# Kernel tuning notes

Hardware: AMD Instinct MI355X
Metric: run time of the kernel (lower is better)

The kernel has to match this reference:

```python
import jax, jax.numpy as jnp
import numpy as np

N = 50000      # nodes
E = 800000     # edges
G = 256        # graphs in batch
D_IN = 128     # input_dim
H = 128        # node_hidden_dim
FC = 128       # fc_hidden_dim
OUT = 2        # out_dim
EPS = 1e-5


def _lin_init(key, fan_in, fan_out, bias=True):
    kw, kb = jax.random.split(key)
    w = jax.random.normal(kw, (fan_in, fan_out), jnp.float32) / np.sqrt(fan_in)
    if bias:
        b = jax.random.normal(kb, (fan_out,), jnp.float32) * 0.01
        return w, b
    return w


def setup_inputs() -> dict:
    key = jax.random.key(0)
    ks = jax.random.split(key, 16)
    x = jax.random.normal(ks[0], (N, D_IN), jnp.float32)
    edge_index = jax.random.randint(ks[1], (2, E), 0, N, jnp.int32)
    batch = jnp.sort(jax.random.randint(ks[2], (N,), 0, G, jnp.int32))
    edge_attr = jax.random.uniform(ks[3], (E, 1), jnp.float32)
    # GraphConv params: lin_rel (with bias) + lin_root (no bias)
    w_rel1, b_rel1 = _lin_init(ks[4], D_IN, H)
    w_root1 = _lin_init(ks[5], D_IN, H, bias=False)
    w_rel2, b_rel2 = _lin_init(ks[6], H, 2 * H)
    w_root2 = _lin_init(ks[7], H, 2 * H, bias=False)
    w_rel3, b_rel3 = _lin_init(ks[8], 2 * H, 3 * H)
    w_root3 = _lin_init(ks[9], 2 * H, 3 * H, bias=False)
    # BatchNorm affine params
    gamma1 = jnp.ones((H,), jnp.float32);      beta1 = jnp.zeros((H,), jnp.float32)
    gamma2 = jnp.ones((2 * H,), jnp.float32);  beta2 = jnp.zeros((2 * H,), jnp.float32)
    gamma3 = jnp.ones((3 * H,), jnp.float32);  beta3 = jnp.zeros((3 * H,), jnp.float32)
    # FC head: lin1 in = 3H+6H+9H = 18H
    w_lin1, b_lin1 = _lin_init(ks[10], 18 * H, FC)
    w_lin2, b_lin2 = _lin_init(ks[11], FC, OUT)
    w_lin3, b_lin3 = _lin_init(ks[12], OUT, OUT)
    return dict(x=x, edge_index=edge_index, batch=batch, edge_attr=edge_attr,
                w_rel1=w_rel1, b_rel1=b_rel1, w_root1=w_root1,
                w_rel2=w_rel2, b_rel2=b_rel2, w_root2=w_root2,
                w_rel3=w_rel3, b_rel3=b_rel3, w_root3=w_root3,
                gamma1=gamma1, beta1=beta1, gamma2=gamma2, beta2=beta2,
                gamma3=gamma3, beta3=beta3,
                w_lin1=w_lin1, b_lin1=b_lin1, w_lin2=w_lin2, b_lin2=b_lin2,
                w_lin3=w_lin3, b_lin3=b_lin3)


def _bn(h, gamma, beta):
    # training-mode BatchNorm1d over node axis
    mu = h.mean(0)
    var = h.var(0)
    return (h - mu) * jax.lax.rsqrt(var + EPS) * gamma + beta


def _gconv(h, src, dst, ew, w_rel, b_rel, w_root):
    # PyG GraphConv: lin_rel(sum_j ew_ij * x_j) + lin_root(x_i)
    agg = jax.ops.segment_sum(h[src] * ew[:, None], dst, num_segments=N)
    return agg @ w_rel + b_rel + h @ w_root


def _pool3(h, batch):
    # concat of global max / mean / add pooling per graph
    s = jax.ops.segment_sum(h, batch, num_segments=G)
    cnt = jax.ops.segment_sum(jnp.ones((h.shape[0], 1), h.dtype), batch, num_segments=G)
    mean = s / jnp.maximum(cnt, 1.0)
    m = jax.ops.segment_max(h, batch, num_segments=G)
    m = jnp.where(cnt > 0, m, 0.0)  # guard empty segments
    return jnp.concatenate([m, mean, s], axis=1)


def reference(x, edge_index, batch, edge_attr,
              w_rel1, b_rel1, w_root1, w_rel2, b_rel2, w_root2,
              w_rel3, b_rel3, w_root3,
              gamma1, beta1, gamma2, beta2, gamma3, beta3,
              w_lin1, b_lin1, w_lin2, b_lin2, w_lin3, b_lin3):
    ew = jnp.transpose(edge_attr, (1, 0))[0]            # [E]
    src, dst = edge_index[0], edge_index[1]
    h = _bn(jax.nn.leaky_relu(_gconv(x, src, dst, ew, w_rel1, b_rel1, w_root1)), gamma1, beta1)
    x1 = _pool3(h, batch)
    h = _bn(jax.nn.leaky_relu(_gconv(h, src, dst, ew, w_rel2, b_rel2, w_root2)), gamma2, beta2)
    x2 = _pool3(h, batch)
    h = _bn(jax.nn.leaky_relu(_gconv(h, src, dst, ew, w_rel3, b_rel3, w_root3)), gamma3, beta3)
    x3 = _pool3(h, batch)
    z = jnp.concatenate([x1, x2, x3], axis=1)           # [G, 18H]
    z = jax.nn.relu(z @ w_lin1 + b_lin1)                # dropout is identity in eval
    z = jax.nn.relu(z @ w_lin2 + b_lin2)
    return jax.nn.log_softmax(z @ w_lin3 + b_lin3, axis=-1)
```

## Files before the change

kernel.cpp:

```cpp
#include <hip/hip_runtime.h>
#include <cstdint>
#include <cstddef>

#define N_NODES 50000
#define M_PAD   50048
#define MB_TILES 391
#define N_EDGES 800000
#define N_GRAPH 256
#define Z_DIM   2304
#define NREP    16
#define POOL_TOT (N_GRAPH * (128 + 256 + 384))

static constexpr float LEAKY  = 0.01f;
static constexpr float BN_EPS = 1e-5f;

typedef short short8 __attribute__((ext_vector_type(8)));
typedef float floatx4 __attribute__((ext_vector_type(4)));
typedef const __attribute__((address_space(1))) unsigned int* gas_ptr;
typedef __attribute__((address_space(3))) unsigned int* las_ptr;
typedef unsigned long long ull;

__device__ __forceinline__ unsigned short f2b(float f) {
  union { float f; unsigned int u; } v; v.f = f;
  unsigned int u = v.u;
  unsigned int r = (u + 0x7FFFu + ((u >> 16) & 1u)) >> 16;
  return (unsigned short)r;
}
__device__ __forceinline__ float b2f(unsigned short h) {
  union { unsigned int u; float f; } v; v.u = ((unsigned int)h) << 16;
  return v.f;
}
__device__ __forceinline__ unsigned fkey(float x) {
  unsigned k = __float_as_uint(x);
  return k ^ ((k & 0x80000000u) ? 0xFFFFFFFFu : 0x80000000u);
}
__device__ __forceinline__ float kdec(unsigned k) {
  k ^= (k & 0x80000000u) ? 0x80000000u : 0xFFFFFFFFu;
  return __uint_as_float(k);
}


__global__ void init_all_kernel(int* __restrict__ cntR, int* __restrict__ gcnt,
                                float* __restrict__ sums_all,
                                unsigned* __restrict__ pmaxk, unsigned* __restrict__ pmink,
                                float* __restrict__ psumg) {
  const int i = blockIdx.x * blockDim.x + threadIdx.x;
  if (i < NREP * N_NODES) cntR[i] = 0;
  if (i < N_GRAPH) gcnt[i] = 0;
  if (i < 2 * (128 + 256 + 384)) sums_all[i] = 0.f;
  if (i < POOL_TOT) { pmaxk[i] = 0u; pmink[i] = 0xFFFFFFFFu; psumg[i] = 0.f; }
}


__global__ void hist_rep_kernel(const int* __restrict__ idx, int* __restrict__ cntR, int n) {
  int i = blockIdx.x * blockDim.x + threadIdx.x;
  if (i < n) {
    const int rep = blockIdx.x & (NREP - 1);
    atomicAdd(&cntR[rep * N_NODES + idx[i]], 1);
  }
}

__global__ __launch_bounds__(256) void scan1_fused_kernel(int* __restrict__ cntR,
                                                          int* __restrict__ out,
                                                          int* __restrict__ part, int n) {
  __shared__ int sm[256];
  const int t = threadIdx.x;
  const int base = blockIdx.x * 1024 + t * 4;
  int v[4] = {0, 0, 0, 0};
#pragma unroll
  for (int j = 0; j < 4; ++j) {
    const int d = base + j;
    if (d < n) {
      int s = 0;
#pragma unroll
      for (int r = 0; r < NREP; ++r) {
        const int c = cntR[r * N_NODES + d];
        cntR[r * N_NODES + d] = s;
        s += c;
      }
      v[j] = s;
    }
  }
  const int tsum = v[0] + v[1] + v[2] + v[3];
  sm[t] = tsum;
  __syncthreads();
  for (int off = 1; off < 256; off <<= 1) {
    int x = (t >= off) ? sm[t - off] : 0;
    __syncthreads();
    sm[t] += x;
    __syncthreads();
  }
  const int excl = sm[t] - tsum;
  if (base     < n) out[base]     = excl;
  if (base + 1 < n) out[base + 1] = excl + v[0];
  if (base + 2 < n) out[base + 2] = excl + v[0] + v[1];
  if (base + 3 < n) out[base + 3] = excl + v[0] + v[1] + v[2];
  if (t == 255) part[blockIdx.x] = sm[255];
}

__global__ __launch_bounds__(256) void scan2_kernel(int* __restrict__ part, int nb,
                                                    int* __restrict__ total_out) {
  __shared__ int sm[256];
  const int t = threadIdx.x;
  const int v = (t < nb) ? part[t] : 0;
  sm[t] = v;
  __syncthreads();
  for (int off = 1; off < 256; off <<= 1) {
    int x = (t >= off) ? sm[t - off] : 0;
    __syncthreads();
    sm[t] += x;
    __syncthreads();
  }
  if (t < nb) part[t] = sm[t] - v;
  if (t == 255) *total_out = sm[255];
}

__global__ void scan3_cursor_kernel(int* __restrict__ out, const int* __restrict__ part,
                                    int* __restrict__ cntR, int n) {
  int i = blockIdx.x * blockDim.x + threadIdx.x;
  if (i >= n) return;
  const int rp = out[i] + part[i >> 10];
  out[i] = rp;
#pragma unroll
  for (int r = 0; r < NREP; ++r) cntR[r * N_NODES + i] += rp;
}

__global__ void bucket_kernel(const int* __restrict__ src, const int* __restrict__ dst,
                              const float* __restrict__ ew, int* __restrict__ cntR,
                              ull* __restrict__ epack, int E) {
  int e = blockIdx.x * blockDim.x + threadIdx.x;
  if (e < E) {
    const int rep = blockIdx.x & (NREP - 1);
    const int d = dst[e];
    const int p = atomicAdd(&cntR[rep * N_NODES + d], 1);
    epack[p] = ((ull)__float_as_uint(ew[e]) << 32) | (unsigned)src[e];
  }
}

__global__ __launch_bounds__(256) void hist_batch_kernel(const int* __restrict__ idx,
                                                         int* __restrict__ cnt, int n) {
  __shared__ int lh[N_GRAPH];
  lh[threadIdx.x] = 0;
  __syncthreads();
  int i = blockIdx.x * blockDim.x + threadIdx.x;
  if (i < n) atomicAdd(&lh[idx[i]], 1);
  __syncthreads();
  const int v = lh[threadIdx.x];
  if (v) atomicAdd(&cnt[threadIdx.x], v);
}

__global__ __launch_bounds__(256) void scan256_kernel(const int* __restrict__ cnt,
                                                      int* __restrict__ gptr) {
  __shared__ int sm[256];
  const int t = threadIdx.x;
  const int v = cnt[t];
  sm[t] = v;
  __syncthreads();
  for (int off = 1; off < 256; off <<= 1) {
    int x = (t >= off) ? sm[t - off] : 0;
    __syncthreads();
    sm[t] += x;
    __syncthreads();
  }
  gptr[t] = sm[t] - v;
  if (t == 255) gptr[256] = sm[255];
}


__global__ void cast_bf16_kernel(const float* __restrict__ in,
                                 unsigned short* __restrict__ out, int npair) {
  int i = blockIdx.x * blockDim.x + threadIdx.x;
  if (i >= npair) return;
  float2 v = *(const float2*)(in + 2 * (size_t)i);
  ((unsigned int*)out)[i] = (unsigned int)f2b(v.x) | ((unsigned int)f2b(v.y) << 16);
}

__global__ __launch_bounds__(256) void wt_build_kernel(
    const float* __restrict__ wrel, const float* __restrict__ wroot,
    const float* __restrict__ brel, const float* __restrict__ sums_prev,
    const float* __restrict__ gamma_prev, const float* __restrict__ beta_prev,
    unsigned short* __restrict__ wt, float* __restrict__ u, float* __restrict__ v,
    int K, int N) {
  __shared__ float redu[256];
  __shared__ float redv[256];
  const int n = blockIdx.x;
  const int K2 = 2 * K;
  const float inv_n = 1.f / (float)N_NODES;
  float us = 0.f, vs = 0.f;
  for (int k = threadIdx.x; k < K2; k += 256) {
    const int kk = (k < K) ? k : k - K;
    const float w = (k < K) ? wrel[(size_t)kk * N + n] : wroot[(size_t)kk * N + n];
    float sc = 1.f, sh = 0.f;
    if (sums_prev) {
      const float mu  = sums_prev[kk] * inv_n;
      const float var = sums_prev[K + kk] * inv_n - mu * mu;
      sc = rsqrtf(var + BN_EPS) * gamma_prev[kk];
      sh = beta_prev[kk] - mu * sc;
    }
    wt[(size_t)n * K2 + k] = f2b(w * sc);
    if (k < K) us += sh * w; else vs += sh * w;
  }
  redu[threadIdx.x] = us; redv[threadIdx.x] = vs;
  __syncthreads();
  for (int o = 128; o > 0; o >>= 1) {
    if (threadIdx.x < o) {
      redu[threadIdx.x] += redu[threadIdx.x + o];
      redv[threadIdx.x] += redv[threadIdx.x + o];
    }
    __syncthreads();
  }
  if (threadIdx.x == 0) { u[n] = redu[0]; v[n] = brel[n] + redv[0]; }
}


template <int D>
__global__ void agg_bf16_kernel(const unsigned short* __restrict__ h,
                                const int* __restrict__ rowptr,
                                const ull* __restrict__ epack,
                                unsigned short* __restrict__ agg,
                                float* __restrict__ degw_out) {
  int gid  = blockIdx.x * blockDim.x + threadIdx.x;
  int node = gid >> 6;
  int lane = threadIdx.x & 63;
  if (node >= N_NODES) return;
  const int beg = rowptr[node], end = rowptr[node + 1];
  constexpr int NP = D / 128;
  float acc0[NP], acc1[NP];
#pragma unroll
  for (int i = 0; i < NP; ++i) { acc0[i] = 0.f; acc1[i] = 0.f; }
  float wsum = 0.f;

  int p = beg;
  for (; p + 4 <= end; p += 4) {
    const ull p0 = epack[p],     p1 = epack[p + 1];
    const ull p2 = epack[p + 2], p3 = epack[p + 3];
    const int s0 = (int)(unsigned)p0, s1 = (int)(unsigned)p1;
    const int s2 = (int)(unsigned)p2, s3 = (int)(unsigned)p3;
    const float w0 = __uint_as_float((unsigned)(p0 >> 32));
    const float w1 = __uint_as_float((unsigned)(p1 >> 32));
    const float w2 = __uint_as_float((unsigned)(p2 >> 32));
    const float w3 = __uint_as_float((unsigned)(p3 >> 32));
    wsum += w0 + w1 + w2 + w3;
    const unsigned int* r0 = (const unsigned int*)(h + (size_t)s0 * D);
    const unsigned int* r1 = (const unsigned int*)(h + (size_t)s1 * D);
    const unsigned int* r2 = (const unsigned int*)(h + (size_t)s2 * D);
    const unsigned int* r3 = (const unsigned int*)(h + (size_t)s3 * D);
    unsigned int u0[NP], u1[NP], u2[NP], u3[NP];
#pragma unroll
    for (int i = 0; i < NP; ++i) {
      u0[i] = r0[lane + 64 * i];
      u1[i] = r1[lane + 64 * i];
      u2[i] = r2[lane + 64 * i];
      u3[i] = r3[lane + 64 * i];
    }
#pragma unroll
    for (int i = 0; i < NP; ++i) {
      acc0[i] += b2f((unsigned short)(u0[i] & 0xFFFF)) * w0
               + b2f((unsigned short)(u1[i] & 0xFFFF)) * w1
               + b2f((unsigned short)(u2[i] & 0xFFFF)) * w2
               + b2f((unsigned short)(u3[i] & 0xFFFF)) * w3;
      acc1[i] += b2f((unsigned short)(u0[i] >> 16)) * w0
               + b2f((unsigned short)(u1[i] >> 16)) * w1
               + b2f((unsigned short)(u2[i] >> 16)) * w2
               + b2f((unsigned short)(u3[i] >> 16)) * w3;
    }
  }
  for (; p < end; ++p) {
    const ull pk = epack[p];
    const int   s = (int)(unsigned)pk;
    const float w = __uint_as_float((unsigned)(pk >> 32));
    wsum += w;
    const unsigned int* row = (const unsigned int*)(h + (size_t)s * D);
#pragma unroll
    for (int i = 0; i < NP; ++i) {
      unsigned int uu = row[lane + 64 * i];
      acc0[i] += b2f((unsigned short)(uu & 0xFFFF)) * w;
      acc1[i] += b2f((unsigned short)(uu >> 16)) * w;
    }
  }
  unsigned int* o = (unsigned int*)(agg + (size_t)node * D);
#pragma unroll
  for (int i = 0; i < NP; ++i)
    o[lane + 64 * i] = (unsigned int)f2b(acc0[i]) | ((unsigned int)f2b(acc1[i]) << 16);
  if (degw_out != nullptr && lane == 0) degw_out[node] = wsum;
}


__global__ __launch_bounds__(256) void gemm_mfma_kernel(
    const unsigned short* __restrict__ Aagg, const unsigned short* __restrict__ Ah,
    const unsigned short* __restrict__ Wt,
    const float* __restrict__ u, const float* __restrict__ v,
    const float* __restrict__ degw,
    unsigned short* __restrict__ outH, float* __restrict__ sums,
    int M, int K, int N) {
  __shared__ unsigned short As[128 * 32];
  __shared__ unsigned short Bs[128 * 32];
  __shared__ float col_s[256];
  __shared__ float dws[128];

  const int NT = N >> 7;
  const int id = blockIdx.x;
  const int xcd = id & 7;
  const int q   = id >> 3;
  const int m_tile = (q / NT) * 8 + xcd;
  if (m_tile >= MB_TILES) return;
  const int m0 = m_tile * 128;
  const int n0 = (q % NT) * 128;

  const int t  = threadIdx.x;
  const int lane = t & 63;
  const int w    = t >> 6;
  const int wm   = (w & 1) * 64;
  const int wn   = (w >> 1) * 64;
  const int l16  = lane & 15;
  const int lq   = lane >> 4;
  const int K2   = 2 * K;

  const int lrow  = lane >> 2;
  const int lslot = lane & 3;

  col_s[t] = 0.f;
  if (t < 128) {
    const int m = m0 + t;
    dws[t] = (m < M) ? degw[m] : 0.f;
  }

  floatx4 acc[4][4];
#pragma unroll
  for (int i = 0; i < 4; ++i)
#pragma unroll
    for (int j = 0; j < 4; ++j) acc[i][j] = (floatx4){0.f, 0.f, 0.f, 0.f};

  for (int k0 = 0; k0 < K2; k0 += 32) {
    const unsigned short* Asrc;
    int kbase;
    if (k0 < K) { Asrc = Aagg; kbase = k0; } else { Asrc = Ah; kbase = k0 - K; }

    __syncthreads();
#pragma unroll
    for (int qq = 0; qq < 2; ++qq) {
      const int row = w * 32 + qq * 16 + lrow;
      const int gc  = (lslot ^ ((row >> 1) & 3)) * 8;
      const unsigned short* gA = Asrc + (size_t)(m0 + row) * K + kbase + gc;
      const unsigned short* gB = Wt + (size_t)(n0 + row) * K2 + k0 + gc;
      __builtin_amdgcn_global_load_lds((gas_ptr)gA, (las_ptr)(As + (w * 32 + qq * 16) * 32),
                                       16, 0, 0);
      __builtin_amdgcn_global_load_lds((gas_ptr)gB, (las_ptr)(Bs + (w * 32 + qq * 16) * 32),
                                       16, 0, 0);
    }
    __syncthreads();

    short8 af[4], bfr[4];
#pragma unroll
    for (int i = 0; i < 4; ++i) {
      const int r = wm + i * 16 + l16;
      af[i] = *(const short8*)(As + r * 32 + (lq ^ ((r >> 1) & 3)) * 8);
    }
#pragma unroll
    for (int j = 0; j < 4; ++j) {
      const int r = wn + j * 16 + l16;
      bfr[j] = *(const short8*)(Bs + r * 32 + (lq ^ ((r >> 1) & 3)) * 8);
    }

#pragma unroll
    for (int i = 0; i < 4; ++i)
#pragma unroll
      for (int j = 0; j < 4; ++j)
        acc[i][j] = __builtin_amdgcn_mfma_f32_16x16x32_bf16(af[i], bfr[j], acc[i][j], 0, 0, 0);
  }

  float uu[4], vv[4];
#pragma unroll
  for (int j = 0; j < 4; ++j) {
    const int n = n0 + wn + j * 16 + l16;
    uu[j] = u[n]; vv[j] = v[n];
  }

  float ts[4]  = {0.f, 0.f, 0.f, 0.f};
  float tss[4] = {0.f, 0.f, 0.f, 0.f};
#pragma unroll
  for (int i = 0; i < 4; ++i) {
    const int lrow2 = wm + i * 16 + lq * 4;
#pragma unroll
    for (int j = 0; j < 4; ++j) {
      const int n = n0 + wn + j * 16 + l16;
#pragma unroll
      for (int r = 0; r < 4; ++r) {
        const int m = m0 + lrow2 + r;
        if (m < M) {
          float val = acc[i][j][r] + vv[j] + dws[lrow2 + r] * uu[j];
          val = val > 0.f ? val : LEAKY * val;
          outH[(size_t)m * N + n] = f2b(val);
          ts[j]  += val;
          tss[j] += val * val;
        }
      }
    }
  }
#pragma unroll
  for (int j = 0; j < 4; ++j) {
    float a = ts[j], b = tss[j];
    a += __shfl_xor(a, 16); a += __shfl_xor(a, 32);
    b += __shfl_xor(b, 16); b += __shfl_xor(b, 32);
    if (lq == 0) {
      const int ci = wn + j * 16 + l16;
      atomicAdd(&col_s[ci], a);
      atomicAdd(&col_s[128 + ci], b);
    }
  }
  __syncthreads();
  if (t < 128) {
    atomicAdd(&sums[n0 + t], col_s[t]);
    atomicAdd(&sums[N + n0 + t], col_s[128 + t]);
  }
}


__global__ void pool_bf16_kernel(const unsigned short* __restrict__ hp,
                                 const int* __restrict__ batch,
                                 unsigned* __restrict__ pmaxk, unsigned* __restrict__ pmink,
                                 float* __restrict__ psumg, int n, int C) {
  __shared__ int bs[64];
  const int tc = threadIdx.x;
  const int r0 = blockIdx.x * 64;
  const int r1 = min(n, r0 + 64);
  if (tc < 64 && r0 + tc < n) bs[tc] = batch[r0 + tc];
  __syncthreads();
  int cur_g = bs[0];
  float mx0 = -3.4e38f, mn0 = 3.4e38f, s0 = 0.f;
  float mx1 = -3.4e38f, mn1 = 3.4e38f, s1 = 0.f;
  for (int r = r0; r < r1; ++r) {
    const int g = bs[r - r0];
    if (g != cur_g) {
      const int c0 = 2 * tc;
      atomicMax(&pmaxk[(size_t)cur_g * C + c0], fkey(mx0));
      atomicMin(&pmink[(size_t)cur_g * C + c0], fkey(mn0));
      atomicAdd(&psumg[(size_t)cur_g * C + c0], s0);
      atomicMax(&pmaxk[(size_t)cur_g * C + c0 + 1], fkey(mx1));
      atomicMin(&pmink[(size_t)cur_g * C + c0 + 1], fkey(mn1));
      atomicAdd(&psumg[(size_t)cur_g * C + c0 + 1], s1);
      mx0 = -3.4e38f; mn0 = 3.4e38f; s0 = 0.f;
      mx1 = -3.4e38f; mn1 = 3.4e38f; s1 = 0.f;
      cur_g = g;
    }
    const unsigned uu = ((const unsigned*)(hp + (size_t)r * C))[tc];
    const float a = b2f((unsigned short)(uu & 0xFFFF));
    const float b = b2f((unsigned short)(uu >> 16));
    mx0 = fmaxf(mx0, a); mn0 = fminf(mn0, a); s0 += a;
    mx1 = fmaxf(mx1, b); mn1 = fminf(mn1, b); s1 += b;
  }
  const int c0 = 2 * tc;
  atomicMax(&pmaxk[(size_t)cur_g * C + c0], fkey(mx0));
  atomicMin(&pmink[(size_t)cur_g * C + c0], fkey(mn0));
  atomicAdd(&psumg[(size_t)cur_g * C + c0], s0);
  atomicMax(&pmaxk[(size_t)cur_g * C + c0 + 1], fkey(mx1));
  atomicMin(&pmink[(size_t)cur_g * C + c0 + 1], fkey(mn1));
  atomicAdd(&psumg[(size_t)cur_g * C + c0 + 1], s1);
}


__global__ void pool_finalize_all_kernel(const unsigned* __restrict__ pmaxk,
                                         const unsigned* __restrict__ pmink,
                                         const float* __restrict__ psumg,
                                         const float* __restrict__ sums_all,
                                         const float* __restrict__ gamma1, const float* __restrict__ beta1,
                                         const float* __restrict__ gamma2, const float* __restrict__ beta2,
                                         const float* __restrict__ gamma3, const float* __restrict__ beta3,
                                         const int* __restrict__ gptr,
                                         float* __restrict__ z) {
  int i = blockIdx.x * blockDim.x + threadIdx.x;
  if (i >= POOL_TOT) return;
  int C, zoff, li;
  const float *sums, *gamma, *beta;
  if (i < N_GRAPH * 128) {
    C = 128; zoff = 0; li = i;
    sums = sums_all; gamma = gamma1; beta = beta1;
  } else if (i < N_GRAPH * (128 + 256)) {
    C = 256; zoff = 384; li = i - N_GRAPH * 128;
    sums = sums_all + 2 * 128; gamma = gamma2; beta = beta2;
  } else {
    C = 384; zoff = 1152; li = i - N_GRAPH * (128 + 256);
    sums = sums_all + 2 * (128 + 256); gamma = gamma3; beta = beta3;
  }
  const int g = li / C, c = li % C;
  const int cnt = gptr[g + 1] - gptr[g];
  const float inv_n = 1.f / (float)N_NODES;
  const float mu  = sums[c] * inv_n;
  const float var = sums[C + c] * inv_n - mu * mu;
  const float sc  = rsqrtf(var + BN_EPS) * gamma[c];
  const float sh  = beta[c] - mu * sc;
  const float mx = kdec(pmaxk[i]);
  const float mn = kdec(pmink[i]);
  const float sm = psumg[i];
  const float zmax = (sc >= 0.f ? mx : mn) * sc + sh;
  const float zsum = sm * sc + (float)cnt * sh;
  float* zg = z + (size_t)g * Z_DIM + zoff;
  zg[c]         = (cnt > 0) ? zmax : 0.f;
  zg[C + c]     = zsum / (float)(cnt > 0 ? cnt : 1);
  zg[2 * C + c] = zsum;
}


__global__ __launch_bounds__(1024) void fc_kernel(const float* __restrict__ z,
                                                  const float* __restrict__ w1, const float* __restrict__ b1,
                                                  const float* __restrict__ w2, const float* __restrict__ b2,
                                                  const float* __restrict__ w3, const float* __restrict__ b3,
                                                  float* __restrict__ out) {
  __shared__ float zs[Z_DIM];
  __shared__ float part[8][128];
  __shared__ float h1s[128];
  __shared__ float red[128][2];
  __shared__ float y2[2];
  const int g  = blockIdx.x;
  const int t  = threadIdx.x;
  const int c  = t & 127;
  const int ks = t >> 7;
  for (int i = t; i < Z_DIM; i += 1024) zs[i] = z[(size_t)g * Z_DIM + i];
  __syncthreads();

  constexpr int KCH = Z_DIM / 8;
  const int k0 = ks * KCH;
  float acc = 0.f;
#pragma unroll 4
  for (int k = k0; k < k0 + KCH; ++k) acc += zs[k] * w1[(size_t)k * 128 + c];
  part[ks][c] = acc;
  __syncthreads();

  if (t < 128) {
    float s = b1[t];
#pragma unroll
    for (int i = 0; i < 8; ++i) s += part[i][t];
    h1s[t] = fmaxf(s, 0.f);
  }
  __syncthreads();
  if (t < 128) {
    red[t][0] = h1s[t] * w2[t * 2 + 0];
    red[t][1] = h1s[t] * w2[t * 2 + 1];
  }
  __syncthreads();
  if (t < 2) {
    float s = b2[t];
    for (int k = 0; k < 128; ++k) s += red[k][t];
    y2[t] = fmaxf(s, 0.f);
  }
  __syncthreads();
  if (t == 0) {
    const float z0 = y2[0] * w3[0] + y2[1] * w3[2] + b3[0];
    const float z1 = y2[0] * w3[1] + y2[1] * w3[3] + b3[1];
    const float m  = fmaxf(z0, z1);
    const float lse = m + logf(expf(z0 - m) + expf(z1 - m));
    out[g * 2 + 0] = z0 - lse;
    out[g * 2 + 1] = z1 - lse;
  }
}


extern "C" void kernel_launch(void* const* d_in, const int* in_sizes, int n_in,
                              void* d_out, int out_size, void* d_ws, size_t ws_size,
                              hipStream_t stream) {
  (void)in_sizes; (void)n_in; (void)out_size; (void)ws_size;
  const float* x        = (const float*)d_in[0];
  const int*   eidx     = (const int*)d_in[1];
  const int*   batch    = (const int*)d_in[2];
  const float* eattr    = (const float*)d_in[3];
  const float* w_rel1   = (const float*)d_in[4];
  const float* b_rel1   = (const float*)d_in[5];
  const float* w_root1  = (const float*)d_in[6];
  const float* w_rel2   = (const float*)d_in[7];
  const float* b_rel2   = (const float*)d_in[8];
  const float* w_root2  = (const float*)d_in[9];
  const float* w_rel3   = (const float*)d_in[10];
  const float* b_rel3   = (const float*)d_in[11];
  const float* w_root3  = (const float*)d_in[12];
  const float* gamma1   = (const float*)d_in[13];
  const float* beta1    = (const float*)d_in[14];
  const float* gamma2   = (const float*)d_in[15];
  const float* beta2    = (const float*)d_in[16];
  const float* gamma3   = (const float*)d_in[17];
  const float* beta3    = (const float*)d_in[18];
  const float* w_lin1   = (const float*)d_in[19];
  const float* b_lin1   = (const float*)d_in[20];
  const float* w_lin2   = (const float*)d_in[21];
  const float* b_lin2   = (const float*)d_in[22];
  const float* w_lin3   = (const float*)d_in[23];
  const float* b_lin3   = (const float*)d_in[24];

  const int* src = eidx;
  const int* dst = eidx + N_EDGES;
  float* outp = (float*)d_out;

  char* ws = (char*)d_ws;
  size_t off = 0;
  auto alloc = [&](size_t bytes) -> void* {
    void* p = ws + off;
    off += (bytes + 255) & ~(size_t)255;
    return p;
  };
  int*   rowptr = (int*)alloc((N_NODES + 1) * sizeof(int));
  int*   cntR   = (int*)alloc((size_t)NREP * N_NODES * sizeof(int));
  int*   gptr   = (int*)alloc((N_GRAPH + 1) * sizeof(int));
  int*   gcnt   = (int*)alloc(N_GRAPH * sizeof(int));
  int*   part   = (int*)alloc(256 * sizeof(int));
  ull*   epack  = (ull*)alloc((size_t)N_EDGES * sizeof(ull));
  float* degw   = (float*)alloc(N_NODES * sizeof(float));
  float* sums_all = (float*)alloc(2 * (128 + 256 + 384) * sizeof(float));
  float* zbuf   = (float*)alloc((size_t)N_GRAPH * Z_DIM * sizeof(float));
  unsigned* pmaxk = (unsigned*)alloc((size_t)POOL_TOT * 4);
  unsigned* pmink = (unsigned*)alloc((size_t)POOL_TOT * 4);
  float*    psumg = (float*)alloc((size_t)POOL_TOT * 4);
  unsigned short* xb   = (unsigned short*)alloc((size_t)M_PAD * 128 * 2);
  unsigned short* hp1  = (unsigned short*)alloc((size_t)M_PAD * 128 * 2);
  unsigned short* hp2  = (unsigned short*)alloc((size_t)M_PAD * 256 * 2);
  unsigned short* hp3  = (unsigned short*)alloc((size_t)M_PAD * 384 * 2);
  unsigned short* aggb = (unsigned short*)alloc((size_t)M_PAD * 256 * 2);
  unsigned short* wt1 = (unsigned short*)alloc((size_t)128 * 256 * 2);
  unsigned short* wt2 = (unsigned short*)alloc((size_t)256 * 256 * 2);
  unsigned short* wt3 = (unsigned short*)alloc((size_t)384 * 512 * 2);
  float* u1 = (float*)alloc(128 * sizeof(float));
  float* v1 = (float*)alloc(128 * sizeof(float));
  float* u2 = (float*)alloc(256 * sizeof(float));
  float* v2 = (float*)alloc(256 * sizeof(float));
  float* u3 = (float*)alloc(384 * sizeof(float));
  float* v3 = (float*)alloc(384 * sizeof(float));

  float* sums1 = sums_all;
  float* sums2 = sums_all + 2 * 128;
  float* sums3 = sums_all + 2 * (128 + 256);
  const int PO1 = 0, PO2 = N_GRAPH * 128, PO3 = N_GRAPH * (128 + 256);

  const int EB = (N_EDGES + 255) / 256;
  const int NB = (N_NODES + 255) / 256;
  const int RB = (N_NODES + 63) / 64;
  const int SB = (N_NODES + 1023) / 1024;

  init_all_kernel<<<(NREP * N_NODES + 255) / 256, 256, 0, stream>>>(
      cntR, gcnt, sums_all, pmaxk, pmink, psumg);

  hist_rep_kernel<<<EB, 256, 0, stream>>>(dst, cntR, N_EDGES);
  scan1_fused_kernel<<<SB, 256, 0, stream>>>(cntR, rowptr, part, N_NODES);
  scan2_kernel<<<1, 256, 0, stream>>>(part, SB, rowptr + N_NODES);
  scan3_cursor_kernel<<<NB, 256, 0, stream>>>(rowptr, part, cntR, N_NODES);
  bucket_kernel<<<EB, 256, 0, stream>>>(src, dst, eattr, cntR, epack, N_EDGES);

  hist_batch_kernel<<<NB, 256, 0, stream>>>(batch, gcnt, N_NODES);
  scan256_kernel<<<1, 256, 0, stream>>>(gcnt, gptr);

  cast_bf16_kernel<<<(N_NODES * 128 / 2 + 255) / 256, 256, 0, stream>>>(x, xb, N_NODES * 128 / 2);
  wt_build_kernel<<<128, 256, 0, stream>>>(w_rel1, w_root1, b_rel1, nullptr, nullptr, nullptr,
                                           wt1, u1, v1, 128, 128);

  const int aggBlocks = (N_NODES * 64 + 255) / 256;

  agg_bf16_kernel<128><<<aggBlocks, 256, 0, stream>>>(xb, rowptr, epack, aggb, degw);
  gemm_mfma_kernel<<<392 * 1, 256, 0, stream>>>(aggb, xb, wt1, u1, v1, degw,
                                                hp1, sums1, N_NODES, 128, 128);
  pool_bf16_kernel<<<RB, 64, 0, stream>>>(hp1, batch, pmaxk + PO1, pmink + PO1, psumg + PO1,
                                          N_NODES, 128);
  wt_build_kernel<<<256, 256, 0, stream>>>(w_rel2, w_root2, b_rel2, sums1, gamma1, beta1,
                                           wt2, u2, v2, 128, 256);

  agg_bf16_kernel<128><<<aggBlocks, 256, 0, stream>>>(hp1, rowptr, epack, aggb, nullptr);
  gemm_mfma_kernel<<<392 * 2, 256, 0, stream>>>(aggb, hp1, wt2, u2, v2, degw,
                                                hp2, sums2, N_NODES, 128, 256);
  pool_bf16_kernel<<<RB, 128, 0, stream>>>(hp2, batch, pmaxk + PO2, pmink + PO2, psumg + PO2,
                                           N_NODES, 256);
  wt_build_kernel<<<384, 256, 0, stream>>>(w_rel3, w_root3, b_rel3, sums2, gamma2, beta2,
                                           wt3, u3, v3, 256, 384);

  agg_bf16_kernel<256><<<aggBlocks, 256, 0, stream>>>(hp2, rowptr, epack, aggb, nullptr);
  gemm_mfma_kernel<<<392 * 3, 256, 0, stream>>>(aggb, hp2, wt3, u3, v3, degw,
                                                hp3, sums3, N_NODES, 256, 384);
  pool_bf16_kernel<<<RB, 192, 0, stream>>>(hp3, batch, pmaxk + PO3, pmink + PO3, psumg + PO3,
                                           N_NODES, 384);

  pool_finalize_all_kernel<<<(POOL_TOT + 255) / 256, 256, 0, stream>>>(
      pmaxk, pmink, psumg, sums_all, gamma1, beta1, gamma2, beta2, gamma3, beta3, gptr, zbuf);
  fc_kernel<<<N_GRAPH, 1024, 0, stream>>>(zbuf, w_lin1, b_lin1, w_lin2, b_lin2, w_lin3, b_lin3,
                                          outp);
}
```

Before: 577.0 us.

## Halve GEMM M-tile to 64 rows and vectorize 256-wide aggregation loads

The fused GEMM now uses 64-row M tiles instead of 128, so it launches twice as many blocks, each holding half the accumulators. This is meant to raise occupancy and balance work across CUs for the 50k-node GEMMs, at the cost of loading the B tile twice as often. The aggregation kernel is split into a 128-wide version and a 256-wide version, and the 256-wide one gathers each row with a single 8-byte uint2 load per lane. That gives wider, contiguous per-lane gathers, though each lane now does more conversion work.

Result: slower. 594.7 us (+3.1%).

```diff
diff --git a/kernel.cpp b/kernel.cpp
--- a/kernel.cpp
+++ b/kernel.cpp
@@ -4,7 +4,7 @@
 
 #define N_NODES 50000
 #define M_PAD   50048
-#define MB_TILES 391
+#define MB64    782
 #define N_EDGES 800000
 #define N_GRAPH 256
 #define Z_DIM   2304
@@ -213,76 +213,96 @@
 }
 
 
-template <int D>
-__global__ void agg_bf16_kernel(const unsigned short* __restrict__ h,
-                                const int* __restrict__ rowptr,
-                                const ull* __restrict__ epack,
-                                unsigned short* __restrict__ agg,
-                                float* __restrict__ degw_out) {
+__global__ void agg128_kernel(const unsigned short* __restrict__ h,
+                              const int* __restrict__ rowptr,
+                              const ull* __restrict__ epack,
+                              unsigned short* __restrict__ agg,
+                              float* __restrict__ degw_out) {
   int gid  = blockIdx.x * blockDim.x + threadIdx.x;
   int node = gid >> 6;
   int lane = threadIdx.x & 63;
   if (node >= N_NODES) return;
   const int beg = rowptr[node], end = rowptr[node + 1];
-  constexpr int NP = D / 128;
-  float acc0[NP], acc1[NP];
-#pragma unroll
-  for (int i = 0; i < NP; ++i) { acc0[i] = 0.f; acc1[i] = 0.f; }
+  float acc0 = 0.f, acc1 = 0.f;
   float wsum = 0.f;
 
   int p = beg;
   for (; p + 4 <= end; p += 4) {
     const ull p0 = epack[p],     p1 = epack[p + 1];
     const ull p2 = epack[p + 2], p3 = epack[p + 3];
-    const int s0 = (int)(unsigned)p0, s1 = (int)(unsigned)p1;
-    const int s2 = (int)(unsigned)p2, s3 = (int)(unsigned)p3;
     const float w0 = __uint_as_float((unsigned)(p0 >> 32));
     const float w1 = __uint_as_float((unsigned)(p1 >> 32));
     const float w2 = __uint_as_float((unsigned)(p2 >> 32));
     const float w3 = __uint_as_float((unsigned)(p3 >> 32));
     wsum += w0 + w1 + w2 + w3;
-    const unsigned int* r0 = (const unsigned int*)(h + (size_t)s0 * D);
-    const unsigned int* r1 = (const unsigned int*)(h + (size_t)s1 * D);
-    const unsigned int* r2 = (const unsigned int*)(h + (size_t)s2 * D);
-    const unsigned int* r3 = (const unsigned int*)(h + (size_t)s3 * D);
-    unsigned int u0[NP], u1[NP], u2[NP], u3[NP];
-#pragma unroll
-    for (int i = 0; i < NP; ++i) {
-      u0[i] = r0[lane + 64 * i];
-      u1[i] = r1[lane + 64 * i];
-      u2[i] = r2[lane + 64 * i];
-      u3[i] = r3[lane + 64 * i];
-    }
-#pragma unroll
-    for (int i = 0; i < NP; ++i) {
-      acc0[i] += b2f((unsigned short)(u0[i] & 0xFFFF)) * w0
-               + b2f((unsigned short)(u1[i] & 0xFFFF)) * w1
-               + b2f((unsigned short)(u2[i] & 0xFFFF)) * w2
-               + b2f((unsigned short)(u3[i] & 0xFFFF)) * w3;
-      acc1[i] += b2f((unsigned short)(u0[i] >> 16)) * w0
-               + b2f((unsigned short)(u1[i] >> 16)) * w1
-               + b2f((unsigned short)(u2[i] >> 16)) * w2
-               + b2f((unsigned short)(u3[i] >> 16)) * w3;
-    }
+    const unsigned u0 = ((const unsigned*)(h + (size_t)(unsigned)p0 * 128))[lane];
+    const unsigned u1 = ((const unsigned*)(h + (size_t)(unsigned)p1 * 128))[lane];
+    const unsigned u2 = ((const unsigned*)(h + (size_t)(unsigned)p2 * 128))[lane];
+    const unsigned u3 = ((const unsigned*)(h + (size_t)(unsigned)p3 * 128))[lane];
+    acc0 += b2f((unsigned short)(u0 & 0xFFFF)) * w0 + b2f((unsigned short)(u1 & 0xFFFF)) * w1
+          + b2f((unsigned short)(u2 & 0xFFFF)) * w2 + b2f((unsigned short)(u3 & 0xFFFF)) * w3;
+    acc1 += b2f((unsigned short)(u0 >> 16)) * w0 + b2f((unsigned short)(u1 >> 16)) * w1
+          + b2f((unsigned short)(u2 >> 16)) * w2 + b2f((unsigned short)(u3 >> 16)) * w3;
   }
   for (; p < end; ++p) {
     const ull pk = epack[p];
-    const int   s = (int)(unsigned)pk;
     const float w = __uint_as_float((unsigned)(pk >> 32));
     wsum += w;
-    const unsigned int* row = (const unsigned int*)(h + (size_t)s * D);
-#pragma unroll
-    for (int i = 0; i < NP; ++i) {
-      unsigned int uu = row[lane + 64 * i];
-      acc0[i] += b2f((unsigned short)(uu & 0xFFFF)) * w;
-      acc1[i] += b2f((unsigned short)(uu >> 16)) * w;
-    }
-  }
-  unsigned int* o = (unsigned int*)(agg + (size_t)node * D);
-#pragma unroll
-  for (int i = 0; i < NP; ++i)
-    o[lane + 64 * i] = (unsigned int)f2b(acc0[i]) | ((unsigned int)f2b(acc1[i]) << 16);
+    const unsigned uu = ((const unsigned*)(h + (size_t)(unsigned)pk * 128))[lane];
+    acc0 += b2f((unsigned short)(uu & 0xFFFF)) * w;
+    acc1 += b2f((unsigned short)(uu >> 16)) * w;
+  }
+  ((unsigned*)(agg + (size_t)node * 128))[lane] =
+      (unsigned)f2b(acc0) | ((unsigned)f2b(acc1) << 16);
   if (degw_out != nullptr && lane == 0) degw_out[node] = wsum;
+}
+
+
+__global__ void agg256_kernel(const unsigned short* __restrict__ h,
+                              const int* __restrict__ rowptr,
+                              const ull* __restrict__ epack,
+                              unsigned short* __restrict__ agg) {
+  int gid  = blockIdx.x * blockDim.x + threadIdx.x;
+  int node = gid >> 6;
+  int lane = threadIdx.x & 63;
+  if (node >= N_NODES) return;
+  const int beg = rowptr[node], end = rowptr[node + 1];
+  float a0 = 0.f, a1 = 0.f, a2 = 0.f, a3 = 0.f;
+
+  int p = beg;
+  for (; p + 4 <= end; p += 4) {
+    const ull p0 = epack[p],     p1 = epack[p + 1];
+    const ull p2 = epack[p + 2], p3 = epack[p + 3];
+    const float w0 = __uint_as_float((unsigned)(p0 >> 32));
+    const float w1 = __uint_as_float((unsigned)(p1 >> 32));
+    const float w2 = __uint_as_float((unsigned)(p2 >> 32));
+    const float w3 = __uint_as_float((unsigned)(p3 >> 32));
+    const uint2 u0 = ((const uint2*)(h + (size_t)(unsigned)p0 * 256))[lane];
+    const uint2 u1 = ((const uint2*)(h + (size_t)(unsigned)p1 * 256))[lane];
+    const uint2 u2 = ((const uint2*)(h + (size_t)(unsigned)p2 * 256))[lane];
+    const uint2 u3 = ((const uint2*)(h + (size_t)(unsigned)p3 * 256))[lane];
+    a0 += b2f((unsigned short)(u0.x & 0xFFFF)) * w0 + b2f((unsigned short)(u1.x & 0xFFFF)) * w1
+        + b2f((unsigned short)(u2.x & 0xFFFF)) * w2 + b2f((unsigned short)(u3.x & 0xFFFF)) * w3;
+    a1 += b2f((unsigned short)(u0.x >> 16)) * w0 + b2f((unsigned short)(u1.x >> 16)) * w1
+        + b2f((unsigned short)(u2.x >> 16)) * w2 + b2f((unsigned short)(u3.x >> 16)) * w3;
+    a2 += b2f((unsigned short)(u0.y & 0xFFFF)) * w0 + b2f((unsigned short)(u1.y & 0xFFFF)) * w1
+        + b2f((unsigned short)(u2.y & 0xFFFF)) * w2 + b2f((unsigned short)(u3.y & 0xFFFF)) * w3;
+    a3 += b2f((unsigned short)(u0.y >> 16)) * w0 + b2f((unsigned short)(u1.y >> 16)) * w1
+        + b2f((unsigned short)(u2.y >> 16)) * w2 + b2f((unsigned short)(u3.y >> 16)) * w3;
+  }
+  for (; p < end; ++p) {
+    const ull pk = epack[p];
+    const float w = __uint_as_float((unsigned)(pk >> 32));
+    const uint2 uu = ((const uint2*)(h + (size_t)(unsigned)pk * 256))[lane];
+    a0 += b2f((unsigned short)(uu.x & 0xFFFF)) * w;
+    a1 += b2f((unsigned short)(uu.x >> 16)) * w;
+    a2 += b2f((unsigned short)(uu.y & 0xFFFF)) * w;
+    a3 += b2f((unsigned short)(uu.y >> 16)) * w;
+  }
+  uint2 o;
+  o.x = (unsigned)f2b(a0) | ((unsigned)f2b(a1) << 16);
+  o.y = (unsigned)f2b(a2) | ((unsigned)f2b(a3) << 16);
+  ((uint2*)(agg + (size_t)node * 256))[lane] = o;
 }
 
 
@@ -293,24 +313,24 @@
     const float* __restrict__ degw,
     unsigned short* __restrict__ outH, float* __restrict__ sums,
     int M, int K, int N) {
-  __shared__ unsigned short As[128 * 32];
+  __shared__ unsigned short As[64 * 32];
   __shared__ unsigned short Bs[128 * 32];
   __shared__ float col_s[256];
-  __shared__ float dws[128];
+  __shared__ float dws[64];
 
   const int NT = N >> 7;
   const int id = blockIdx.x;
   const int xcd = id & 7;
   const int q   = id >> 3;
   const int m_tile = (q / NT) * 8 + xcd;
-  if (m_tile >= MB_TILES) return;
-  const int m0 = m_tile * 128;
+  if (m_tile >= MB64) return;
+  const int m0 = m_tile * 64;
   const int n0 = (q % NT) * 128;
 
   const int t  = threadIdx.x;
   const int lane = t & 63;
   const int w    = t >> 6;
-  const int wm   = (w & 1) * 64;
+  const int wm   = (w & 1) * 32;
   const int wn   = (w >> 1) * 64;
   const int l16  = lane & 15;
   const int lq   = lane >> 4;
@@ -320,14 +340,14 @@
   const int lslot = lane & 3;
 
   col_s[t] = 0.f;
-  if (t < 128) {
+  if (t < 64) {
     const int m = m0 + t;
     dws[t] = (m < M) ? degw[m] : 0.f;
   }
 
-  floatx4 acc[4][4];
-#pragma unroll
-  for (int i = 0; i < 4; ++i)
+  floatx4 acc[2][4];
+#pragma unroll
+  for (int i = 0; i < 2; ++i)
 #pragma unroll
     for (int j = 0; j < 4; ++j) acc[i][j] = (floatx4){0.f, 0.f, 0.f, 0.f};
 
@@ -337,22 +357,25 @@
     if (k0 < K) { Asrc = Aagg; kbase = k0; } else { Asrc = Ah; kbase = k0 - K; }
 
     __syncthreads();
+    {
+      const int row = w * 16 + lrow;
+      const int gc  = (lslot ^ ((row >> 1) & 3)) * 8;
+      const unsigned short* gA = Asrc + (size_t)(m0 + row) * K + kbase + gc;
+      __builtin_amdgcn_global_load_lds((gas_ptr)gA, (las_ptr)(As + (w * 16) * 32), 16, 0, 0);
+    }
 #pragma unroll
     for (int qq = 0; qq < 2; ++qq) {
       const int row = w * 32 + qq * 16 + lrow;
       const int gc  = (lslot ^ ((row >> 1) & 3)) * 8;
-      const unsigned short* gA = Asrc + (size_t)(m0 + row) * K + kbase + gc;
       const unsigned short* gB = Wt + (size_t)(n0 + row) * K2 + k0 + gc;
-      __builtin_amdgcn_global_load_lds((gas_ptr)gA, (las_ptr)(As + (w * 32 + qq * 16) * 32),
-                                       16, 0, 0);
       __builtin_amdgcn_global_load_lds((gas_ptr)gB, (las_ptr)(Bs + (w * 32 + qq * 16) * 32),
                                        16, 0, 0);
     }
     __syncthreads();
 
-    short8 af[4], bfr[4];
-#pragma unroll
-    for (int i = 0; i < 4; ++i) {
+    short8 af[2], bfr[4];
+#pragma unroll
+    for (int i = 0; i < 2; ++i) {
       const int r = wm + i * 16 + l16;
       af[i] = *(const short8*)(As + r * 32 + (lq ^ ((r >> 1) & 3)) * 8);
     }
@@ -363,7 +386,7 @@
     }
 
 #pragma unroll
-    for (int i = 0; i < 4; ++i)
+    for (int i = 0; i < 2; ++i)
 #pragma unroll
       for (int j = 0; j < 4; ++j)
         acc[i][j] = __builtin_amdgcn_mfma_f32_16x16x32_bf16(af[i], bfr[j], acc[i][j], 0, 0, 0);
@@ -379,7 +402,7 @@
   float ts[4]  = {0.f, 0.f, 0.f, 0.f};
   float tss[4] = {0.f, 0.f, 0.f, 0.f};
 #pragma unroll
-  for (int i = 0; i < 4; ++i) {
+  for (int i = 0; i < 2; ++i) {
     const int lrow2 = wm + i * 16 + lq * 4;
 #pragma unroll
     for (int j = 0; j < 4; ++j) {
@@ -632,6 +655,7 @@
   const int NB = (N_NODES + 255) / 256;
   const int RB = (N_NODES + 63) / 64;
   const int SB = (N_NODES + 1023) / 1024;
+  const int GEMM_MB = 98 * 8;
 
   init_all_kernel<<<(NREP * N_NODES + 255) / 256, 256, 0, stream>>>(
       cntR, gcnt, sums_all, pmaxk, pmink, psumg);
@@ -651,25 +675,25 @@
 
   const int aggBlocks = (N_NODES * 64 + 255) / 256;
 
-  agg_bf16_kernel<128><<<aggBlocks, 256, 0, stream>>>(xb, rowptr, epack, aggb, degw);
-  gemm_mfma_kernel<<<392 * 1, 256, 0, stream>>>(aggb, xb, wt1, u1, v1, degw,
-                                                hp1, sums1, N_NODES, 128, 128);
+  agg128_kernel<<<aggBlocks, 256, 0, stream>>>(xb, rowptr, epack, aggb, degw);
+  gemm_mfma_kernel<<<GEMM_MB * 1, 256, 0, stream>>>(aggb, xb, wt1, u1, v1, degw,
+                                                    hp1, sums1, N_NODES, 128, 128);
   pool_bf16_kernel<<<RB, 64, 0, stream>>>(hp1, batch, pmaxk + PO1, pmink + PO1, psumg + PO1,
                                           N_NODES, 128);
   wt_build_kernel<<<256, 256, 0, stream>>>(w_rel2, w_root2, b_rel2, sums1, gamma1, beta1,
                                            wt2, u2, v2, 128, 256);
 
-  agg_bf16_kernel<128><<<aggBlocks, 256, 0, stream>>>(hp1, rowptr, epack, aggb, nullptr);
-  gemm_mfma_kernel<<<392 * 2, 256, 0, stream>>>(aggb, hp1, wt2, u2, v2, degw,
-                                                hp2, sums2, N_NODES, 128, 256);
+  agg128_kernel<<<aggBlocks, 256, 0, stream>>>(hp1, rowptr, epack, aggb, nullptr);
+  gemm_mfma_kernel<<<GEMM_MB * 2, 256, 0, stream>>>(aggb, hp1, wt2, u2, v2, degw,
+                                                    hp2, sums2, N_NODES, 128, 256);
   pool_bf16_kernel<<<RB, 128, 0, stream>>>(hp2, batch, pmaxk + PO2, pmink + PO2, psumg + PO2,
                                            N_NODES, 256);
   wt_build_kernel<<<384, 256, 0, stream>>>(w_rel3, w_root3, b_rel3, sums2, gamma2, beta2,
                                            wt3, u3, v3, 256, 384);
 
-  agg_bf16_kernel<256><<<aggBlocks, 256, 0, stream>>>(hp2, rowptr, epack, aggb, nullptr);
-  gemm_mfma_kernel<<<392 * 3, 256, 0, stream>>>(aggb, hp2, wt3, u3, v3, degw,
-                                                hp3, sums3, N_NODES, 256, 384);
+  agg256_kernel<<<aggBlocks, 256, 0, stream>>>(hp2, rowptr, epack, aggb);
+  gemm_mfma_kernel<<<GEMM_MB * 3, 256, 0, stream>>>(aggb, hp2, wt3, u3, v3, degw,
+                                                    hp3, sums3, N_NODES, 256, 384);
   pool_bf16_kernel<<<RB, 192, 0, stream>>>(hp3, batch, pmaxk + PO3, pmink + PO3, psumg + PO3,
                                            N_NODES, 384);
 
```
